# Optimization experiments

Measured on AMD Instinct MI355X. Metric: run time of the kernel, lower is better.

## Reference

```python
import jax, jax.numpy as jnp
import numpy as np
import math

D_MODEL = 256
D_STATE = 16
DT_RANK = math.ceil(D_MODEL / 16)  # 16
WINDOW = 8
B, S = 2, 1024
LN_EPS = 1e-5


def setup_inputs() -> dict:
    key = jax.random.key(0)
    ks = jax.random.split(key, 24)
    d, n, r = D_MODEL, D_STATE, DT_RANK
    sc = lambda fan_in: 1.0 / math.sqrt(fan_in)
    inp = {
        "x": jax.random.normal(ks[0], (B, S, d), jnp.float32),
        # SelectiveSSM params
        "A_log": jnp.log(jnp.abs(jax.random.normal(ks[1], (d, n))) + 1e-4),
        "W_xproj": jax.random.normal(ks[2], (d, r + n)) * sc(d),
        "W_dt": jax.random.normal(ks[3], (r, d)) * sc(r),
        "b_dt": jnp.zeros((d,)),
        "W_C": jax.random.normal(ks[4], (d, n)) * sc(d),
        # LinearAttentionPathway params
        "Wq": jax.random.normal(ks[5], (d, d)) * sc(d),
        "Wk": jax.random.normal(ks[6], (d, d)) * sc(d),
        "Wv": jax.random.normal(ks[7], (d, d)) * sc(d),
        "Wo": jax.random.normal(ks[8], (d, d)) * sc(d),
        "omega": jax.random.normal(ks[9], (d, d)) * 0.5,  # RFF frequencies (buffer)
        # EntropyGate net: Linear(2d+1 -> d), SiLU, Linear(d -> d), Sigmoid
        "Wg1": jax.random.normal(ks[10], (2 * d + 1, d)) * sc(2 * d + 1),
        "bg1": jnp.zeros((d,)),
        "Wg2": jax.random.normal(ks[11], (d, d)) * sc(d),
        "bg2": jnp.zeros((d,)),
        # LayerNorms
        "ln1_g": jnp.ones((d,)), "ln1_b": jnp.zeros((d,)),
        "ln2_g": jnp.ones((d,)), "ln2_b": jnp.zeros((d,)),
        # FFN (dropout is identity in eval)
        "Wf1": jax.random.normal(ks[12], (d, 4 * d)) * sc(d),
        "bf1": jnp.zeros((4 * d,)),
        "Wf2": jax.random.normal(ks[13], (4 * d, d)) * sc(4 * d),
        "bf2": jnp.zeros((d,)),
    }
    return inp


def _layernorm(x, g, b):
    mu = jnp.mean(x, axis=-1, keepdims=True)
    var = jnp.mean((x - mu) ** 2, axis=-1, keepdims=True)
    return (x - mu) / jnp.sqrt(var + LN_EPS) * g + b


def _ssm(x, A_log, W_xproj, W_dt, b_dt, W_C):
    b, s, d = x.shape
    A = -jnp.exp(A_log)                                   # (d, n)
    xp = x @ W_xproj                                      # (b, s, r+n)
    delta = jax.nn.softplus(xp[..., :DT_RANK] @ W_dt + b_dt)  # (b, s, d)
    Bt = xp[..., DT_RANK:]                                # (b, s, n)
    Ct = x @ W_C                                          # (b, s, n)

    def step(h, ins):
        dlt, B_, C_, x_ = ins                             # (b,d),(b,n),(b,n),(b,d)
        A_bar = jnp.exp(dlt[..., None] * A)               # (b, d, n)
        h = A_bar * h + (dlt * x_)[..., None] * B_[:, None, :]
        y = jnp.einsum('bn,bdn->bd', C_, h)
        return h, y

    xs = (delta.transpose(1, 0, 2), Bt.transpose(1, 0, 2),
          Ct.transpose(1, 0, 2), x.transpose(1, 0, 2))
    h0 = jnp.zeros((b, d, D_STATE), x.dtype)
    _, ys = jax.lax.scan(step, h0, xs)                    # (s, b, d)
    return ys.transpose(1, 0, 2)


def _rff(x, omega):
    proj = x @ omega
    scale = math.sqrt(2.0 / D_MODEL)
    return scale * jnp.concatenate([jnp.cos(proj), jnp.sin(proj)], axis=-1)


def _linear_attn(x, Wq, Wk, Wv, Wo, omega):
    b, s, d = x.shape
    Qp = _rff(x @ Wq, omega)                              # (b, s, 2d)
    Kp = _rff(x @ Wk, omega)                              # (b, s, 2d)
    V = x @ Wv                                            # (b, s, d)
    f = 2 * d

    def step(carry, ins):
        Sm, Z = carry                                     # (b,f,d), (b,f)
        q, k, v = ins
        Sm = Sm + k[..., None] * v[:, None, :]
        Z = Z + k
        num = jnp.einsum('bf,bfd->bd', q, Sm)
        den = jnp.sum(q * Z, axis=-1, keepdims=True)
        return (Sm, Z), num / (den + 1e-6)

    xs = (Qp.transpose(1, 0, 2), Kp.transpose(1, 0, 2), V.transpose(1, 0, 2))
    carry0 = (jnp.zeros((b, f, d), x.dtype), jnp.zeros((b, f), x.dtype))
    _, ys = jax.lax.scan(step, carry0, xs)                # (s, b, d)
    return ys.transpose(1, 0, 2) @ Wo


def _entropy(x):
    # H_t over trailing window of token L2-norms; softmax over window.
    m = jnp.linalg.norm(x, axis=-1)                       # (b, s)
    mp = jnp.pad(m, ((0, 0), (WINDOW - 1, 0)), constant_values=-jnp.inf)
    s = m.shape[1]
    # windows[b, t, w]: norms of positions t-W+1..t (padded with -inf)
    windows = jnp.stack([mp[:, i:i + s] for i in range(WINDOW)], axis=-1)
    p = jax.nn.softmax(windows, axis=-1)                  # -inf pads -> p=0
    H = -jnp.sum(p * (jnp.log(p + 1e-9) / jnp.log(2.0)), axis=-1, keepdims=True)
    return H                                              # (b, s, 1)


def reference(x, A_log, W_xproj, W_dt, b_dt, W_C, Wq, Wk, Wv, Wo, omega,
              Wg1, bg1, Wg2, bg2, ln1_g, ln1_b, ln2_g, ln2_b,
              Wf1, bf1, Wf2, bf2):
    residual = x
    y_ssm = _ssm(x, A_log, W_xproj, W_dt, b_dt, W_C)
    y_attn = _linear_attn(x, Wq, Wk, Wv, Wo, omega)
    H = _entropy(x)
    gate_in = jnp.concatenate([y_ssm, y_attn, H], axis=-1)
    g = jax.nn.sigmoid(jax.nn.silu(gate_in @ Wg1 + bg1) @ Wg2 + bg2)
    y_gated = g * y_ssm + (1.0 - g) * y_attn
    h = _layernorm(residual + y_gated, ln1_g, ln1_b)
    ffn = jax.nn.gelu(h @ Wf1 + bf1, approximate=False) @ Wf2 + bf2
    return _layernorm(h + ffn, ln2_g, ln2_b)
```

## Files before the change

### kernel.cpp

```cpp
#include <hip/hip_runtime.h>
#include <math.h>

typedef unsigned short ushort_t;
typedef unsigned int uint_t;
typedef __attribute__((ext_vector_type(8))) short short8;
typedef __attribute__((ext_vector_type(4))) float f32x4;

#define ACT_NONE     0
#define ACT_SOFTPLUS 1
#define ACT_SILU     2
#define ACT_SIGMOID  3
#define ACT_GELU     4
#define ACT_RFF      5
#define ACT_CAUSAL   6

__device__ __forceinline__ ushort_t f2b(float f) {
    union { float f; uint_t u; } v; v.f = f;
    uint_t u = v.u;
    uint_t r = (u + 0x7FFFu + ((u >> 16) & 1u)) >> 16;
    return (ushort_t)r;
}
__device__ __forceinline__ float b2f(ushort_t h) {
    union { uint_t u; float f; } v; v.u = ((uint_t)h) << 16;
    return v.f;
}
__device__ __forceinline__ void split2(float v, ushort_t& h0, ushort_t& h1) {
    h0 = f2b(v); h1 = f2b(v - b2f(h0));
}
__device__ __forceinline__ void split3(float v, ushort_t& h0, ushort_t& h1, ushort_t& h2) {
    h0 = f2b(v); float r1 = v - b2f(h0);
    h1 = f2b(r1); h2 = f2b(r1 - b2f(h1));
}

__device__ __forceinline__ float fast_erf(float x) {
    float ax = fabsf(x);
    float t = 1.f / (1.f + 0.3275911f * ax);
    float poly = t * (0.254829592f + t * (-0.284496736f + t * (1.421413741f
               + t * (-1.453152027f + t * 1.061405429f))));
    float er = 1.f - poly * __expf(-ax * ax);
    return copysignf(er, x);
}

__device__ __forceinline__ float act_apply(float v, int act) {
    switch (act) {
        case ACT_SOFTPLUS: return v > 0.f ? v + __logf(1.f + __expf(-v)) : __logf(1.f + __expf(v));
        case ACT_SILU:     return v / (1.f + __expf(-v));
        case ACT_SIGMOID:  return 1.f / (1.f + __expf(-v));
        case ACT_GELU:     return 0.5f * v * (1.f + fast_erf(v * 0.7071067811865475f));
        default:           return v;
    }
}

#define LDK2 72
#define TSTRIDE 66

struct GJob {
    const ushort_t *A0, *A1, *A2, *B0, *B1, *B2;
    const float* bias;
    float* outF;
    ushort_t *o0, *o1, *o2, *t0, *t1;
    int lda, ldb, ldo, ldob, colOffB, act, ns, K, N;
    int nx, ny, base, zmod;
    int sAb1, sAb2, sBb1, sBb2, sOb, sObB, sTb;
};

template<int NSMAX>
__global__ __launch_bounds__(256)
void gemm_multi(GJob J0, GJob J1, GJob J2, GJob J3, GJob J4)
{
    __shared__ ushort_t sA[NSMAX][64 * LDK2];
    __shared__ ushort_t sB[NSMAX][64 * LDK2];

    GJob J = J0;
    int bid = blockIdx.x;
    if (J4.nx && bid >= J4.base) J = J4;
    else if (J3.nx && bid >= J3.base) J = J3;
    else if (J2.nx && bid >= J2.base) J = J2;
    else if (J1.nx && bid >= J1.base) J = J1;

    int rel = bid - J.base;
    int perz = J.nx * J.ny;
    int bz = rel / perz; rel -= bz * perz;
    int by = rel / J.nx, bx = rel - by * J.nx;
    int zq = bz / J.zmod, zr = bz - zq * J.zmod;

    const ushort_t* As[3] = {J.A0, J.A1, J.A2};
    const ushort_t* Bs[3] = {J.B0, J.B1, J.B2};
    long offA = (long)zq * J.sAb1 + (long)zr * J.sAb2;
    long offB = (long)zq * J.sBb1 + (long)zr * J.sBb2;
    #pragma unroll
    for (int s = 0; s < NSMAX; ++s) { As[s] += offA; Bs[s] += offB; }
    float* outF = J.outF ? J.outF + (long)bz * J.sOb : nullptr;
    ushort_t* o0 = J.o0 ? J.o0 + (long)bz * J.sObB : nullptr;
    ushort_t* o1 = J.o1 ? J.o1 + (long)bz * J.sObB : nullptr;
    ushort_t* o2 = J.o2 ? J.o2 + (long)bz * J.sObB : nullptr;

    const int m0 = by * 64, n0 = bx * 64;
    const int tid = threadIdx.x, lane = tid & 63, wid = tid >> 6;
    const int wr = (wid >> 1) * 32, wc = (wid & 1) * 32;
    const int lr = lane & 15, lk = (lane >> 4) * 8;
    const int rS = tid >> 3, c8 = (tid & 7) * 8;

    uint4 rA[NSMAX][2], rB[NSMAX][2];

    auto LOAD = [&](int k0) {
        #pragma unroll
        for (int s = 0; s < NSMAX; ++s) if (s < J.ns) {
            #pragma unroll
            for (int p = 0; p < 2; ++p) {
                rA[s][p] = *(const uint4*)(As[s] + (long)(m0 + rS + 32 * p) * J.lda + k0 + c8);
                rB[s][p] = *(const uint4*)(Bs[s] + (long)(n0 + rS + 32 * p) * J.ldb + k0 + c8);
            }
        }
    };
    auto STORE = [&]() {
        #pragma unroll
        for (int s = 0; s < NSMAX; ++s) if (s < J.ns) {
            #pragma unroll
            for (int p = 0; p < 2; ++p) {
                *(uint4*)&sA[s][(rS + 32 * p) * LDK2 + c8] = rA[s][p];
                *(uint4*)&sB[s][(rS + 32 * p) * LDK2 + c8] = rB[s][p];
            }
        }
    };

    f32x4 acc[2][2];
    #pragma unroll
    for (int i = 0; i < 2; ++i)
        #pragma unroll
        for (int j = 0; j < 2; ++j)
            acc[i][j] = (f32x4){0.f, 0.f, 0.f, 0.f};

    const int niter = J.K >> 6;
    LOAD(0);
    for (int it = 0; it < niter; ++it) {
        if (it) __syncthreads();
        STORE();
        __syncthreads();
        if (it + 1 < niter) LOAD((it + 1) << 6);
        #pragma unroll
        for (int ks = 0; ks < 2; ++ks) {
            short8 af[NSMAX][2], bg[NSMAX][2];
            #pragma unroll
            for (int s = 0; s < NSMAX; ++s) if (s < J.ns) {
                af[s][0] = *(const short8*)&sA[s][(wr + lr) * LDK2 + ks * 32 + lk];
                af[s][1] = *(const short8*)&sA[s][(wr + 16 + lr) * LDK2 + ks * 32 + lk];
                bg[s][0] = *(const short8*)&sB[s][(wc + lr) * LDK2 + ks * 32 + lk];
                bg[s][1] = *(const short8*)&sB[s][(wc + 16 + lr) * LDK2 + ks * 32 + lk];
            }
            #pragma unroll
            for (int i = 0; i < 2; ++i) {
                #pragma unroll
                for (int j = 0; j < 2; ++j) {
                    acc[i][j] = __builtin_amdgcn_mfma_f32_16x16x32_bf16(af[0][i], bg[0][j], acc[i][j], 0, 0, 0);
                    if constexpr (NSMAX >= 2) if (J.ns >= 2) {
                        acc[i][j] = __builtin_amdgcn_mfma_f32_16x16x32_bf16(af[0][i], bg[1][j], acc[i][j], 0, 0, 0);
                        acc[i][j] = __builtin_amdgcn_mfma_f32_16x16x32_bf16(af[1][i], bg[0][j], acc[i][j], 0, 0, 0);
                    }
                    if constexpr (NSMAX >= 3) if (J.ns >= 3) {
                        acc[i][j] = __builtin_amdgcn_mfma_f32_16x16x32_bf16(af[0][i], bg[2][j], acc[i][j], 0, 0, 0);
                        acc[i][j] = __builtin_amdgcn_mfma_f32_16x16x32_bf16(af[1][i], bg[1][j], acc[i][j], 0, 0, 0);
                        acc[i][j] = __builtin_amdgcn_mfma_f32_16x16x32_bf16(af[2][i], bg[0][j], acc[i][j], 0, 0, 0);
                    }
                }
            }
        }
    }

    ushort_t* sAf = &sA[0][0];
    ushort_t* sBf = &sB[0][0];
    const bool hasT = (J.t0 != nullptr);
    if (hasT) __syncthreads();

    #pragma unroll
    for (int i = 0; i < 2; ++i) {
        #pragma unroll
        for (int j = 0; j < 2; ++j) {
            #pragma unroll
            for (int rr = 0; rr < 4; ++rr) {
                int rl2 = wr + i * 16 + (lane >> 4) * 4 + rr;
                int cl2 = wc + j * 16 + lr;
                int row = m0 + rl2;
                int col = n0 + cl2;
                if (col >= J.N) continue;
                float v = acc[i][j][rr];
                if (J.bias) v += J.bias[col];
                if (J.act == ACT_RFF) {
                    const float sc = 0.08838834764831845f;
                    float sv_, cv_;
                    __sincosf(v, &sv_, &cv_);
                    float cv = sc * cv_, sv = sc * sv_;
                    ushort_t ch = f2b(cv), sh = f2b(sv);
                    ushort_t cL = f2b(cv - b2f(ch)), sL = f2b(sv - b2f(sh));
                    long oc = (long)row * J.ldob + col, os = oc + J.N;
                    o0[oc] = ch; o0[os] = sh;
                    o1[oc] = cL; o1[os] = sL;
                    if (hasT) {
                        sAf[cl2 * TSTRIDE + rl2] = ch;
                        sAf[4224 + cl2 * TSTRIDE + rl2] = cL;
                        sBf[cl2 * TSTRIDE + rl2] = sh;
                        sBf[4224 + cl2 * TSTRIDE + rl2] = sL;
                    }
                    continue;
                }
                if (J.act == ACT_CAUSAL) { if (col > row) v = 0.f; }
                else v = act_apply(v, J.act);
                if (outF) outF[(long)row * J.ldo + col] = v;
                if (o0) {
                    long o = (long)row * J.ldob + J.colOffB + col;
                    ushort_t h0 = f2b(v); o0[o] = h0;
                    if (o1) {
                        float r1 = v - b2f(h0);
                        ushort_t h1 = f2b(r1); o1[o] = h1;
                        if (o2) o2[o] = f2b(r1 - b2f(h1));
                    }
                }
                if (hasT) {
                    ushort_t h0 = f2b(v);
                    sAf[cl2 * TSTRIDE + rl2] = h0;
                    sAf[4224 + cl2 * TSTRIDE + rl2] = f2b(v - b2f(h0));
                }
            }
        }
    }

    if (hasT) {
        __syncthreads();
        int bb = m0 >> 10, tl0 = m0 & 1023;
        int cl = tid >> 2, seg = tid & 3;
        int ngroups = (J.act == ACT_RFF) ? 2 : 1;
        for (int g = 0; g < ngroups; ++g) {
            const ushort_t* th = (g ? sBf : sAf) + cl * TSTRIDE + seg * 16;
            const ushort_t* tl = th + 4224;
            long gcol = (long)(n0 + cl) + (long)g * J.N;
            long addr = (long)bb * J.sTb + gcol * 1024 + tl0 + seg * 16;
            uint_t wh[8], wl[8];
            #pragma unroll
            for (int k2 = 0; k2 < 8; ++k2) {
                wh[k2] = (uint_t)th[2 * k2] | ((uint_t)th[2 * k2 + 1] << 16);
                wl[k2] = (uint_t)tl[2 * k2] | ((uint_t)tl[2 * k2 + 1] << 16);
            }
            *(uint4*)(J.t0 + addr)     = *(uint4*)&wh[0];
            *(uint4*)(J.t0 + addr + 8) = *(uint4*)&wh[4];
            *(uint4*)(J.t1 + addr)     = *(uint4*)&wl[0];
            *(uint4*)(J.t1 + addr + 8) = *(uint4*)&wl[4];
        }
    }
}

#define CONV_BLKS 6400
__global__ __launch_bounds__(256)
void convert_kernel(const float* __restrict__ x, const float* __restrict__ Wxp,
                    const float* __restrict__ Wdt, const float* __restrict__ Wc,
                    const float* __restrict__ Wq, const float* __restrict__ Wk,
                    const float* __restrict__ Wv, const float* __restrict__ Wo,
                    const float* __restrict__ omega, const float* __restrict__ Wg1,
                    const float* __restrict__ Wg2, const float* __restrict__ Wf1,
                    const float* __restrict__ Wf2,
                    ushort_t* x0, ushort_t* x1, ushort_t* x2,
                    ushort_t* omT0, ushort_t* omT1, ushort_t* omT2,
                    ushort_t* Wq0, ushort_t* Wq1, ushort_t* Wq2,
                    ushort_t* Wk0, ushort_t* Wk1, ushort_t* Wk2,
                    ushort_t* WvT0, ushort_t* WvT1, ushort_t* WoT0, ushort_t* WoT1,
                    ushort_t* Wg1T0, ushort_t* Wg1T1, ushort_t* Wg2T0, ushort_t* Wg2T1,
                    ushort_t* Wf1T, ushort_t* Wf2T,
                    ushort_t* WdtT0, ushort_t* WdtT1, ushort_t* WxpP0, ushort_t* WxpP1,
                    ushort_t* WbcT0, ushort_t* WbcT1, float* mbuf)
{
    if (blockIdx.x >= CONV_BLKS) {
        int w = threadIdx.x >> 6, lane = threadIdx.x & 63;
        int token = (blockIdx.x - CONV_BLKS) * 4 + w;
        const float4 v = ((const float4*)(x + (long)token * 256))[lane];
        float s = v.x * v.x + v.y * v.y + v.z * v.z + v.w * v.w;
        #pragma unroll
        for (int msk = 32; msk; msk >>= 1) s += __shfl_xor(s, msk, 64);
        if (lane == 0) mbuf[token] = sqrtf(s);
        return;
    }
    int i = blockIdx.x * 256 + threadIdx.x;
    if (i < 524288) { split3(x[i], x0[i], x1[i], x2[i]); return; }
    i -= 524288;
    if (i < 65536) { int r = i >> 8, c = i & 255; split3(omega[c * 256 + r], omT0[i], omT1[i], omT2[i]); return; }
    i -= 65536;
    if (i < 65536) { split3(Wq[i], Wq0[i], Wq1[i], Wq2[i]); return; }
    i -= 65536;
    if (i < 65536) { split3(Wk[i], Wk0[i], Wk1[i], Wk2[i]); return; }
    i -= 65536;
    if (i < 65536) { int r = i >> 8, c = i & 255; split2(Wv[c * 256 + r], WvT0[i], WvT1[i]); return; }
    i -= 65536;
    if (i < 65536) { int r = i >> 8, c = i & 255; split2(Wo[c * 256 + r], WoT0[i], WoT1[i]); return; }
    i -= 65536;
    if (i < 147456) { int r = i / 576, c = i - r * 576;
                      float v = (c < 513) ? Wg1[c * 256 + r] : 0.f;
                      split2(v, Wg1T0[i], Wg1T1[i]); return; }
    i -= 147456;
    if (i < 65536) { int r = i >> 8, c = i & 255; split2(Wg2[c * 256 + r], Wg2T0[i], Wg2T1[i]); return; }
    i -= 65536;
    if (i < 262144) { int r = i >> 8, c = i & 255; Wf1T[i] = f2b(Wf1[c * 1024 + r]); return; }
    i -= 262144;
    if (i < 262144) { int r = i >> 10, c = i & 1023; Wf2T[i] = f2b(Wf2[c * 256 + r]); return; }
    i -= 262144;
    if (i < 16384) { int m = i >> 6, k = i & 63;
                     float v = (k < 16) ? Wdt[k * 256 + m] : 0.f;
                     split2(v, WdtT0[i], WdtT1[i]); return; }
    i -= 16384;
    if (i < 16384) { int n = i >> 6, k = i & 63;
                     float v = (k < 16) ? Wxp[n * 32 + k] : 0.f;
                     split2(v, WxpP0[i], WxpP1[i]); return; }
    i -= 16384;
    if (i < 16384) { int r = i >> 8, c = i & 255;
                     float v = (r < 16) ? Wxp[c * 32 + 16 + r] : ((r < 32) ? Wc[c * 16 + (r - 16)] : 0.f);
                     split2(v, WbcT0[i], WbcT1[i]); return; }
}

template<int PASS>
__global__ __launch_bounds__(256)
void ssm_pass(const float* __restrict__ x, const float* __restrict__ delta,
              const float* __restrict__ BtCt, const float* __restrict__ A_log,
              float* __restrict__ hend, float* __restrict__ Pst,
              const float* __restrict__ hstart,
              ushort_t* __restrict__ giH, ushort_t* __restrict__ giL)
{
    __shared__ float sd[64][16], sx[64][16], sB[64][16], sC[64][16];
    const int bx = blockIdx.x;
    const int dblk = bx & 15, c = (bx >> 4) & 15, b = bx >> 8;
    const int tid = threadIdx.x;
    const int n = tid & 15, dl = tid >> 4;
    const int d = dblk * 16 + dl;
    #pragma unroll
    for (int it = 0; it < 4; ++it) {
        int i = it * 256 + tid;
        int t = i >> 4, j = i & 15;
        long row = (long)b * 1024 + c * 64 + t;
        sd[t][j] = delta[row * 256 + dblk * 16 + j];
        sx[t][j] = x[row * 256 + dblk * 16 + j];
        sB[t][j] = BtCt[row * 32 + j];
        if (PASS == 3) sC[t][j] = BtCt[row * 32 + 16 + j];
    }
    __syncthreads();
    const float acoef = -__expf(A_log[d * 16 + n]);
    float h = 0.f, P = 1.f;
    if (PASS == 3) h = hstart[((long)(b * 16 + c) << 12) + d * 16 + n];
    for (int t = 0; t < 64; ++t) {
        float dlt = sd[t][dl];
        float a = __expf(dlt * acoef);
        h = a * h + (dlt * sx[t][dl]) * sB[t][n];
        if (PASS == 1) P *= a;
        if (PASS == 3) {
            float part = sC[t][n] * h;
            #pragma unroll
            for (int msk = 8; msk; msk >>= 1) part += __shfl_xor(part, msk, 16);
            if (n == 0) {
                long row = (long)b * 1024 + c * 64 + t;
                ushort_t hh = f2b(part);
                giH[row * 576 + d] = hh;
                giL[row * 576 + d] = f2b(part - b2f(hh));
            }
        }
    }
    if (PASS == 1) {
        long idx = ((long)(b * 16 + c) << 12) + d * 16 + n;
        hend[idx] = h;
        Pst[idx] = P;
    }
}

__global__ void ssm_scan_kernel(const float* __restrict__ hend,
                                const float* __restrict__ Pst,
                                float* __restrict__ hstart,
                                const ushort_t* __restrict__ Kh,
                                const ushort_t* __restrict__ Kl,
                                float* __restrict__ dzc)
{
    int gb = blockIdx.x;
    if (gb < 32) {
        int tid = gb * 256 + threadIdx.x;
        int b = tid >> 12;
        int dn = tid & 4095;
        float hs = 0.f;
        for (int c = 0; c < 16; ++c) {
            long idx = ((long)(b * 16 + c) << 12) + dn;
            hstart[idx] = hs;
            hs = Pst[idx] * hs + hend[idx];
        }
    } else {
        int idx = (gb - 32) * 256 + threadIdx.x;
        int bc = idx >> 9, f = idx & 511;
        float s = 0.f;
        for (int t = 0; t < 128; ++t) {
            long i = ((long)bc * 128 + t) * 512 + f;
            s += b2f(Kh[i]) + b2f(Kl[i]);
        }
        dzc[(long)bc * 512 + f] = s;
    }
}

__global__ void sscan_kernel(const float* __restrict__ dST,
                             ushort_t* __restrict__ STh, ushort_t* __restrict__ STl)
{
    int t = blockIdx.x * 256 + threadIdx.x;
    int b = t >> 17;
    int df = t & 131071;
    float acc = 0.f;
    for (int c = 0; c < 8; ++c) {
        long idx = (long)(b * 8 + c) * 131072 + df;
        ushort_t h = f2b(acc);
        STh[idx] = h;
        STl[idx] = f2b(acc - b2f(h));
        acc += dST[idx];
    }
}

__global__ void attn_finish(const float* __restrict__ scores,
                            const ushort_t* __restrict__ Qh, const ushort_t* __restrict__ Ql,
                            const float* __restrict__ dzc,
                            const float* __restrict__ numA, const float* __restrict__ numB,
                            const float* __restrict__ mbuf,
                            ushort_t* __restrict__ yh, ushort_t* __restrict__ yl,
                            ushort_t* __restrict__ giH, ushort_t* __restrict__ giL)
{
    int token = blockIdx.x;
    int b = token >> 10, tloc = token & 1023;
    int c = tloc >> 7, tin = tloc & 127;
    int bc = b * 8 + c;
    int lane = threadIdx.x;
    const float* srow = scores + ((long)bc * 128 + tin) * 128;
    float s = srow[lane] + srow[lane + 64];
    const ushort_t* qh = Qh + (long)token * 512;
    const ushort_t* ql = Ql + (long)token * 512;
    float q[8];
    #pragma unroll
    for (int j = 0; j < 8; ++j) {
        int f = lane + 64 * j;
        q[j] = b2f(qh[f]) + b2f(ql[f]);
    }
    for (int c2 = 0; c2 < c; ++c2) {
        const float* z = dzc + (long)(b * 8 + c2) * 512;
        #pragma unroll
        for (int j = 0; j < 8; ++j) s += q[j] * z[lane + 64 * j];
    }
    #pragma unroll
    for (int m = 32; m; m >>= 1) s += __shfl_xor(s, m, 64);
    float inv = 1.f / (s + 1e-6f);
    const float* na = numA + (long)token * 256;
    const float* nb = numB + (long)token * 256;
    #pragma unroll
    for (int j = 0; j < 4; ++j) {
        int idx = lane + 64 * j;
        float v = (na[idx] + nb[idx]) * inv;
        ushort_t h = f2b(v);
        yh[(long)token * 256 + idx] = h;
        yl[(long)token * 256 + idx] = f2b(v - b2f(h));
    }
    if (lane == 0) {
        float w[8];
        #pragma unroll
        for (int i = 0; i < 8; ++i) {
            int idx = tloc - 7 + i;
            w[i] = (idx >= 0) ? mbuf[b * 1024 + idx] : -1e30f;
        }
        float mx = w[0];
        #pragma unroll
        for (int i = 1; i < 8; ++i) mx = fmaxf(mx, w[i]);
        float e[8], sum = 0.f;
        #pragma unroll
        for (int i = 0; i < 8; ++i) { e[i] = __expf(w[i] - mx); sum += e[i]; }
        float invs = 1.f / sum, Hv = 0.f;
        #pragma unroll
        for (int i = 0; i < 8; ++i) {
            float p = e[i] * invs;
            Hv -= p * __logf(p + 1e-9f);
        }
        float H = Hv * 1.4426950408889634f;
        ushort_t hh = f2b(H);
        giH[(long)token * 576 + 512] = hh;
        giL[(long)token * 576 + 512] = f2b(H - b2f(hh));
    }
    if (lane < 63) {
        giH[(long)token * 576 + 513 + lane] = 0;
        giL[(long)token * 576 + 513 + lane] = 0;
    }
}

__global__ __launch_bounds__(256)
void ln1_kernel(const float* __restrict__ x, const float* __restrict__ g,
                const ushort_t* __restrict__ giH, const ushort_t* __restrict__ giL,
                const float* __restrict__ gamma, const float* __restrict__ beta,
                float* __restrict__ outF, ushort_t* __restrict__ outB)
{
    __shared__ float red[8];
    long t = blockIdx.x;
    int i = threadIdx.x;
    long idx = t * 256 + i;
    float yssm  = b2f(giH[t * 576 + i])       + b2f(giL[t * 576 + i]);
    float yattn = b2f(giH[t * 576 + 256 + i]) + b2f(giL[t * 576 + 256 + i]);
    float gv = g[idx];
    float v = x[idx] + gv * yssm + (1.f - gv) * yattn;
    float s = v;
    #pragma unroll
    for (int m = 32; m; m >>= 1) s += __shfl_xor(s, m, 64);
    if ((i & 63) == 0) red[i >> 6] = s;
    __syncthreads();
    float mu = (red[0] + red[1] + red[2] + red[3]) * (1.f / 256.f);
    float dv = v - mu;
    float s2 = dv * dv;
    #pragma unroll
    for (int m = 32; m; m >>= 1) s2 += __shfl_xor(s2, m, 64);
    if ((i & 63) == 0) red[4 + (i >> 6)] = s2;
    __syncthreads();
    float var = (red[4] + red[5] + red[6] + red[7]) * (1.f / 256.f);
    float o = dv * rsqrtf(var + 1e-5f) * gamma[i] + beta[i];
    outF[idx] = o;
    outB[idx] = f2b(o);
}

__global__ __launch_bounds__(256)
void ln2_kernel(const float* __restrict__ h, const float* __restrict__ f2,
                const float* __restrict__ gamma, const float* __restrict__ beta,
                float* __restrict__ out)
{
    __shared__ float red[8];
    long t = blockIdx.x;
    int i = threadIdx.x;
    long idx = t * 256 + i;
    float v = h[idx] + f2[idx];
    float s = v;
    #pragma unroll
    for (int m = 32; m; m >>= 1) s += __shfl_xor(s, m, 64);
    if ((i & 63) == 0) red[i >> 6] = s;
    __syncthreads();
    float mu = (red[0] + red[1] + red[2] + red[3]) * (1.f / 256.f);
    float dv = v - mu;
    float s2 = dv * dv;
    #pragma unroll
    for (int m = 32; m; m >>= 1) s2 += __shfl_xor(s2, m, 64);
    if ((i & 63) == 0) red[4 + (i >> 6)] = s2;
    __syncthreads();
    float var = (red[4] + red[5] + red[6] + red[7]) * (1.f / 256.f);
    out[idx] = dv * rsqrtf(var + 1e-5f) * gamma[i] + beta[i];
}


extern "C" void kernel_launch(void* const* d_in, const int* in_sizes, int n_in,
                              void* d_out, int out_size, void* d_ws, size_t ws_size,
                              hipStream_t stream)
{
    const float* x       = (const float*)d_in[0];
    const float* A_log   = (const float*)d_in[1];
    const float* W_xproj = (const float*)d_in[2];
    const float* W_dt    = (const float*)d_in[3];
    const float* b_dt    = (const float*)d_in[4];
    const float* W_C     = (const float*)d_in[5];
    const float* Wq      = (const float*)d_in[6];
    const float* Wk      = (const float*)d_in[7];
    const float* Wv      = (const float*)d_in[8];
    const float* Wo      = (const float*)d_in[9];
    const float* omega   = (const float*)d_in[10];
    const float* Wg1     = (const float*)d_in[11];
    const float* bg1     = (const float*)d_in[12];
    const float* Wg2     = (const float*)d_in[13];
    const float* bg2     = (const float*)d_in[14];
    const float* ln1_g   = (const float*)d_in[15];
    const float* ln1_b   = (const float*)d_in[16];
    const float* ln2_g   = (const float*)d_in[17];
    const float* ln2_b   = (const float*)d_in[18];
    const float* Wf1     = (const float*)d_in[19];
    const float* bf1     = (const float*)d_in[20];
    const float* Wf2     = (const float*)d_in[21];
    const float* bf2     = (const float*)d_in[22];

    char* B = (char*)d_ws;
    float* out = (float*)d_out;
    if (ws_size < (size_t)36216832) return;

    ushort_t* x0      = (ushort_t*)(B + 0);
    ushort_t* x1      = (ushort_t*)(B + 1048576);
    ushort_t* x2      = (ushort_t*)(B + 2097152);
    ushort_t* Qp_hi   = (ushort_t*)(B + 3145728);
    ushort_t* Qp_lo   = (ushort_t*)(B + 5242880);
    ushort_t* Kp_hi   = (ushort_t*)(B + 7340032);
    ushort_t* Kp_lo   = (ushort_t*)(B + 9437184);
    ushort_t* KpT_hi  = (ushort_t*)(B + 11534336);
    ushort_t* KpT_lo  = (ushort_t*)(B + 13631488);
    ushort_t* VT_hi   = (ushort_t*)(B + 15728640);
    ushort_t* VT_lo   = (ushort_t*)(B + 16777216);
    float*    dST_f   = (float*)(B + 17825792);
    float*    delta_f = (float*)(B + 26214400);
    float*    BtCt_f  = (float*)(B + 28311552);
    ushort_t* Wg1T0   = (ushort_t*)(B + 28573696);
    ushort_t* Wg1T1   = (ushort_t*)(B + 28868608);
    ushort_t* Wf1T    = (ushort_t*)(B + 29163520);
    ushort_t* Wf2T    = (ushort_t*)(B + 29687808);
    ushort_t* WxdT0   = (ushort_t*)(B + 30212096);
    ushort_t* WxdT1   = (ushort_t*)(B + 30343168);
    ushort_t* WvT0    = (ushort_t*)(B + 30474240);
    ushort_t* WvT1    = (ushort_t*)(B + 30605312);
    ushort_t* WoT0    = (ushort_t*)(B + 30736384);
    ushort_t* WoT1    = (ushort_t*)(B + 30867456);
    ushort_t* Wg2T0   = (ushort_t*)(B + 30998528);
    ushort_t* Wg2T1   = (ushort_t*)(B + 31129600);
    ushort_t* WdtT0   = (ushort_t*)(B + 31260672);
    ushort_t* WdtT1   = (ushort_t*)(B + 31293440);
    ushort_t* WxpP0   = (ushort_t*)(B + 31326208);
    ushort_t* WxpP1   = (ushort_t*)(B + 31358976);
    ushort_t* WbcT0   = (ushort_t*)(B + 31391744);
    ushort_t* WbcT1   = (ushort_t*)(B + 31424512);
    float*    mbuf    = (float*)(B + 31457280);
    float*    dzc     = (float*)(B + 31465472);
    ushort_t* gatein_hi = (ushort_t*)(B + 31498240);
    ushort_t* gatein_lo = (ushort_t*)(B + 33857536);
    ushort_t* omT0  = (ushort_t*)(B + 17825792);
    ushort_t* omT1  = (ushort_t*)(B + 17956864);
    ushort_t* omT2  = (ushort_t*)(B + 18087936);
    ushort_t* Wq0   = (ushort_t*)(B + 18219008);
    ushort_t* Wq1   = (ushort_t*)(B + 18350080);
    ushort_t* Wq2   = (ushort_t*)(B + 18481152);
    ushort_t* Wk0   = (ushort_t*)(B + 18612224);
    ushort_t* Wk1   = (ushort_t*)(B + 18743296);
    ushort_t* Wk2   = (ushort_t*)(B + 18874368);
    ushort_t* WqoT0 = (ushort_t*)(B + 19005440);
    ushort_t* WqoT1 = (ushort_t*)(B + 19136512);
    ushort_t* WqoT2 = (ushort_t*)(B + 19267584);
    ushort_t* WkoT0 = (ushort_t*)(B + 19398656);
    ushort_t* WkoT1 = (ushort_t*)(B + 19529728);
    ushort_t* WkoT2 = (ushort_t*)(B + 19660800);
    ushort_t* ST_hi = (ushort_t*)(B + 11534336);
    ushort_t* ST_lo = (ushort_t*)(B + 7340032);
    float*    hend   = (float*)(B + 0);
    float*    Pst    = (float*)(B + 524288);
    float*    hstart = (float*)(B + 1048576);
    float*    scores_f  = (float*)(B + 26214400);
    ushort_t* scores_hi = (ushort_t*)(B + 27262976);
    ushort_t* scores_lo = (ushort_t*)(B + 27787264);
    float*    numA_f = (float*)(B + 17825792);
    float*    numB_f = (float*)(B + 19922944);
    ushort_t* g1_hi  = (ushort_t*)(B + 22020096);
    ushort_t* g1_lo  = (ushort_t*)(B + 23068672);
    float*    gbuf_f = (float*)(B + 24117248);
    ushort_t* ypre_hi = (ushort_t*)(B + 7340032);
    ushort_t* ypre_lo = (ushort_t*)(B + 8388608);
    float*    hbuf_f  = (float*)(B + 11534336);
    ushort_t* hbuf_b  = (ushort_t*)(B + 13631488);
    ushort_t* ffn1_b  = (ushort_t*)(B + 3145728);
    float*    ffn2_f  = (float*)(B + 15728640);

    dim3 T256(256);
    GJob jz{};

    convert_kernel<<<dim3(CONV_BLKS + 512), T256, 0, stream>>>(x, W_xproj, W_dt, W_C,
        Wq, Wk, Wv, Wo, omega, Wg1, Wg2, Wf1, Wf2,
        x0, x1, x2, omT0, omT1, omT2, Wq0, Wq1, Wq2, Wk0, Wk1, Wk2,
        WvT0, WvT1, WoT0, WoT1, Wg1T0, Wg1T1, Wg2T0, Wg2T1, Wf1T, Wf2T,
        WdtT0, WdtT1, WxpP0, WxpP1, WbcT0, WbcT1, mbuf);

    {
        GJob a{}; a.A0=omT0; a.A1=omT1; a.A2=omT2; a.B0=Wq0; a.B1=Wq1; a.B2=Wq2;
        a.o0=WqoT0; a.o1=WqoT1; a.o2=WqoT2; a.lda=256; a.ldb=256; a.ldob=256;
        a.act=ACT_NONE; a.ns=3; a.K=256; a.N=256; a.nx=4; a.ny=4; a.base=0; a.zmod=1;
        GJob b = a; b.B0=Wk0; b.B1=Wk1; b.B2=Wk2; b.o0=WkoT0; b.o1=WkoT1; b.o2=WkoT2; b.base=16;
        GJob c{}; c.A0=WdtT0; c.A1=WdtT1; c.B0=WxpP0; c.B1=WxpP1;
        c.o0=WxdT0; c.o1=WxdT1; c.lda=64; c.ldb=64; c.ldob=256;
        c.act=ACT_NONE; c.ns=2; c.K=64; c.N=256; c.nx=4; c.ny=4; c.base=32; c.zmod=1;
        gemm_multi<3><<<dim3(48), T256, 0, stream>>>(a, b, c, jz, jz);
    }
    {
        GJob v{}; v.A0=x0; v.A1=x1; v.B0=WvT0; v.B1=WvT1;
        v.t0=VT_hi; v.t1=VT_lo; v.sTb=262144;
        v.lda=256; v.ldb=256; v.act=ACT_NONE; v.ns=2; v.K=256; v.N=256;
        v.nx=4; v.ny=32; v.base=0; v.zmod=1;
        GJob q{}; q.A0=x0; q.A1=x1; q.A2=x2; q.B0=WqoT0; q.B1=WqoT1; q.B2=WqoT2;
        q.o0=Qp_hi; q.o1=Qp_lo; q.lda=256; q.ldb=256; q.ldob=512;
        q.act=ACT_RFF; q.ns=3; q.K=256; q.N=256; q.nx=4; q.ny=32; q.base=128; q.zmod=1;
        GJob k = q; k.B0=WkoT0; k.B1=WkoT1; k.B2=WkoT2; k.o0=Kp_hi; k.o1=Kp_lo;
        k.t0=KpT_hi; k.t1=KpT_lo; k.sTb=524288; k.base=256;
        GJob bc{}; bc.A0=x0; bc.A1=x1; bc.B0=WbcT0; bc.B1=WbcT1;
        bc.outF=BtCt_f; bc.lda=256; bc.ldb=256; bc.ldo=32;
        bc.act=ACT_NONE; bc.ns=2; bc.K=256; bc.N=32; bc.nx=1; bc.ny=32; bc.base=384; bc.zmod=1;
        GJob dl{}; dl.A0=x0; dl.A1=x1; dl.B0=WxdT0; dl.B1=WxdT1; dl.bias=b_dt;
        dl.outF=delta_f; dl.lda=256; dl.ldb=256; dl.ldo=256;
        dl.act=ACT_SOFTPLUS; dl.ns=2; dl.K=256; dl.N=256; dl.nx=4; dl.ny=32; dl.base=416; dl.zmod=1;
        gemm_multi<3><<<dim3(544), T256, 0, stream>>>(v, q, k, bc, dl);
    }
    ssm_pass<1><<<dim3(512), T256, 0, stream>>>(x, delta_f, BtCt_f, A_log, hend, Pst, nullptr, nullptr, nullptr);
    ssm_scan_kernel<<<dim3(64), T256, 0, stream>>>(hend, Pst, hstart, Kp_hi, Kp_lo, dzc);
    ssm_pass<3><<<dim3(512), T256, 0, stream>>>(x, delta_f, BtCt_f, A_log, nullptr, nullptr, hstart, gatein_hi, gatein_lo);

    {
        GJob d{}; d.A0=VT_hi; d.A1=VT_lo; d.B0=KpT_hi; d.B1=KpT_lo;
        d.outF=dST_f; d.lda=1024; d.ldb=1024; d.ldo=512;
        d.act=ACT_NONE; d.ns=2; d.K=128; d.N=512; d.nx=8; d.ny=4; d.base=0; d.zmod=8;
        d.sAb1=262144; d.sAb2=128; d.sBb1=524288; d.sBb2=128; d.sOb=131072;
        GJob s{}; s.A0=Qp_hi; s.A1=Qp_lo; s.B0=Kp_hi; s.B1=Kp_lo;
        s.outF=scores_f; s.o0=scores_hi; s.o1=scores_lo;
        s.lda=512; s.ldb=512; s.ldo=128; s.ldob=128;
        s.act=ACT_CAUSAL; s.ns=2; s.K=512; s.N=128; s.nx=2; s.ny=2; s.base=512; s.zmod=1;
        s.sAb1=65536; s.sBb1=65536; s.sOb=16384; s.sObB=16384;
        gemm_multi<2><<<dim3(576), T256, 0, stream>>>(d, s, jz, jz, jz);
    }
    sscan_kernel<<<dim3(1024), T256, 0, stream>>>(dST_f, ST_hi, ST_lo);

    {
        GJob a{}; a.A0=scores_hi; a.A1=scores_lo; a.B0=VT_hi; a.B1=VT_lo;
        a.outF=numA_f; a.lda=128; a.ldb=1024; a.ldo=256;
        a.act=ACT_NONE; a.ns=2; a.K=128; a.N=256; a.nx=4; a.ny=2; a.base=0; a.zmod=8;
        a.sAb1=131072; a.sAb2=16384; a.sBb1=262144; a.sBb2=128; a.sOb=32768;
        GJob b{}; b.A0=Qp_hi; b.A1=Qp_lo; b.B0=ST_hi; b.B1=ST_lo;
        b.outF=numB_f; b.lda=512; b.ldb=512; b.ldo=256;
        b.act=ACT_NONE; b.ns=2; b.K=512; b.N=256; b.nx=4; b.ny=2; b.base=128; b.zmod=1;
        b.sAb1=65536; b.sBb1=131072; b.sOb=32768;
        gemm_multi<2><<<dim3(256), T256, 0, stream>>>(a, b, jz, jz, jz);
    }
    attn_finish<<<dim3(2048), dim3(64), 0, stream>>>(scores_f, Qp_hi, Qp_lo, dzc,
        numA_f, numB_f, mbuf, ypre_hi, ypre_lo, gatein_hi, gatein_lo);

    {
        GJob w{}; w.A0=ypre_hi; w.A1=ypre_lo; w.B0=WoT0; w.B1=WoT1;
        w.o0=gatein_hi; w.o1=gatein_lo; w.colOffB=256;
        w.lda=256; w.ldb=256; w.ldob=576;
        w.act=ACT_NONE; w.ns=2; w.K=256; w.N=256; w.nx=4; w.ny=32; w.base=0; w.zmod=1;
        gemm_multi<2><<<dim3(128), T256, 0, stream>>>(w, jz, jz, jz, jz);
    }
    {
        GJob g{}; g.A0=gatein_hi; g.A1=gatein_lo; g.B0=Wg1T0; g.B1=Wg1T1; g.bias=bg1;
        g.o0=g1_hi; g.o1=g1_lo; g.lda=576; g.ldb=576; g.ldob=256;
        g.act=ACT_SILU; g.ns=2; g.K=576; g.N=256; g.nx=4; g.ny=32; g.base=0; g.zmod=1;
        gemm_multi<2><<<dim3(128), T256, 0, stream>>>(g, jz, jz, jz, jz);
    }
    {
        GJob g{}; g.A0=g1_hi; g.A1=g1_lo; g.B0=Wg2T0; g.B1=Wg2T1; g.bias=bg2;
        g.outF=gbuf_f; g.lda=256; g.ldb=256; g.ldo=256;
        g.act=ACT_SIGMOID; g.ns=2; g.K=256; g.N=256; g.nx=4; g.ny=32; g.base=0; g.zmod=1;
        gemm_multi<2><<<dim3(128), T256, 0, stream>>>(g, jz, jz, jz, jz);
    }
    ln1_kernel<<<dim3(2048), T256, 0, stream>>>(x, gbuf_f, gatein_hi, gatein_lo, ln1_g, ln1_b, hbuf_f, hbuf_b);
    {
        GJob f{}; f.A0=hbuf_b; f.B0=Wf1T; f.bias=bf1;
        f.o0=ffn1_b; f.lda=256; f.ldb=256; f.ldob=1024;
        f.act=ACT_GELU; f.ns=1; f.K=256; f.N=1024; f.nx=16; f.ny=32; f.base=0; f.zmod=1;
        gemm_multi<1><<<dim3(512), T256, 0, stream>>>(f, jz, jz, jz, jz);
    }
    {
        GJob f{}; f.A0=ffn1_b; f.B0=Wf2T; f.bias=bf2;
        f.outF=ffn2_f; f.lda=1024; f.ldb=1024; f.ldo=256;
        f.act=ACT_NONE; f.ns=1; f.K=1024; f.N=256; f.nx=4; f.ny=32; f.base=0; f.zmod=1;
        gemm_multi<1><<<dim3(128), T256, 0, stream>>>(f, jz, jz, jz, jz);
    }
    ln2_kernel<<<dim3(2048), T256, 0, stream>>>(hbuf_f, ffn2_f, ln2_g, ln2_b, out);
}
```

Measured before the change: 329.4 us.

## Fold SSM chunk passes into attention GEMM launches and merge scan kernels

Moves the two SSM chunk-scan passes into extra blocks of the independent attention GEMM launches (pass 1 with the dST/scores GEMM, pass 3 with the numA/numB GEMM), and merges the SSM state scan, dzc reduction and ST prefix scan into one kernel. This cuts four kernel launches and lets the latency-bound sequential SSM blocks run alongside GEMM blocks. To avoid aliasing between concurrently running work, the scores and ST_lo buffers move to new workspace regions, which raises the required workspace size. The price is a larger combined kernel with shared LDS sizing and heterogeneous blocks.

```diff
diff --git a/kernel.cpp b/kernel.cpp
--- a/kernel.cpp
+++ b/kernel.cpp
@@ -64,15 +64,75 @@
     int sAb1, sAb2, sBb1, sBb2, sOb, sObB, sTb;
 };
 
-template<int NSMAX>
+struct SJob {
+    const float *x, *delta, *BtCt, *A_log, *hstart;
+    float *hend, *Pst;
+    ushort_t *giH, *giL;
+    int base;
+};
+
+template<int NSMAX, int AUXPASS>
 __global__ __launch_bounds__(256)
-void gemm_multi(GJob J0, GJob J1, GJob J2, GJob J3, GJob J4)
+void gemm_multi(GJob J0, GJob J1, GJob J2, GJob J3, GJob J4, SJob S)
 {
-    __shared__ ushort_t sA[NSMAX][64 * LDK2];
-    __shared__ ushort_t sB[NSMAX][64 * LDK2];
+    __shared__ ushort_t ldsbuf[NSMAX * 2 * 64 * LDK2];
+    ushort_t (*sA)[64 * LDK2] = (ushort_t(*)[64 * LDK2])ldsbuf;
+    ushort_t (*sB)[64 * LDK2] = (ushort_t(*)[64 * LDK2])(ldsbuf + NSMAX * 64 * LDK2);
+
+    int bid = blockIdx.x;
+
+    if constexpr (AUXPASS != 0) {
+        if (bid >= S.base) {
+            const int bx2 = bid - S.base;
+            const int dblk = bx2 & 15, cc = (bx2 >> 4) & 15, bb2 = bx2 >> 8;
+            const int tid2 = threadIdx.x;
+            const int nn = tid2 & 15, dl = tid2 >> 4;
+            const int dd = dblk * 16 + dl;
+            float* sd  = (float*)ldsbuf;
+            float* sx2 = sd + 1024;
+            float* sB2 = sx2 + 1024;
+            float* sC2 = sB2 + 1024;
+            #pragma unroll
+            for (int it = 0; it < 4; ++it) {
+                int i2 = it * 256 + tid2;
+                int t2 = i2 >> 4, j2 = i2 & 15;
+                long row = (long)bb2 * 1024 + cc * 64 + t2;
+                sd[t2 * 16 + j2]  = S.delta[row * 256 + dblk * 16 + j2];
+                sx2[t2 * 16 + j2] = S.x[row * 256 + dblk * 16 + j2];
+                sB2[t2 * 16 + j2] = S.BtCt[row * 32 + j2];
+                if (AUXPASS == 3) sC2[t2 * 16 + j2] = S.BtCt[row * 32 + 16 + j2];
+            }
+            __syncthreads();
+            const float acoef = -__expf(S.A_log[dd * 16 + nn]);
+            float h = 0.f, P = 1.f;
+            if (AUXPASS == 3) h = S.hstart[((long)(bb2 * 16 + cc) << 12) + dd * 16 + nn];
+            for (int t2 = 0; t2 < 64; ++t2) {
+                float dlt = sd[t2 * 16 + dl];
+                float a2 = __expf(dlt * acoef);
+                h = a2 * h + (dlt * sx2[t2 * 16 + dl]) * sB2[t2 * 16 + nn];
+                if (AUXPASS == 1) P *= a2;
+                if (AUXPASS == 3) {
+                    float part = sC2[t2 * 16 + nn] * h;
+                    #pragma unroll
+                    for (int msk = 8; msk; msk >>= 1) part += __shfl_xor(part, msk, 16);
+                    if (nn == 0) {
+                        long row = (long)bb2 * 1024 + cc * 64 + t2;
+                        ushort_t hh = f2b(part);
+                        S.giH[row * 576 + dd] = hh;
+                        S.giL[row * 576 + dd] = f2b(part - b2f(hh));
+                    }
+                }
+            }
+            if (AUXPASS == 1) {
+                long idx = ((long)(bb2 * 16 + cc) << 12) + dd * 16 + nn;
+                S.hend[idx] = h;
+                S.Pst[idx] = P;
+            }
+            return;
+        }
+    }
 
     GJob J = J0;
-    int bid = blockIdx.x;
     if (J4.nx && bid >= J4.base) J = J4;
     else if (J3.nx && bid >= J3.base) J = J3;
     else if (J2.nx && bid >= J2.base) J = J2;
@@ -313,64 +373,12 @@
                      split2(v, WbcT0[i], WbcT1[i]); return; }
 }
 
-template<int PASS>
-__global__ __launch_bounds__(256)
-void ssm_pass(const float* __restrict__ x, const float* __restrict__ delta,
-              const float* __restrict__ BtCt, const float* __restrict__ A_log,
-              float* __restrict__ hend, float* __restrict__ Pst,
-              const float* __restrict__ hstart,
-              ushort_t* __restrict__ giH, ushort_t* __restrict__ giL)
-{
-    __shared__ float sd[64][16], sx[64][16], sB[64][16], sC[64][16];
-    const int bx = blockIdx.x;
-    const int dblk = bx & 15, c = (bx >> 4) & 15, b = bx >> 8;
-    const int tid = threadIdx.x;
-    const int n = tid & 15, dl = tid >> 4;
-    const int d = dblk * 16 + dl;
-    #pragma unroll
-    for (int it = 0; it < 4; ++it) {
-        int i = it * 256 + tid;
-        int t = i >> 4, j = i & 15;
-        long row = (long)b * 1024 + c * 64 + t;
-        sd[t][j] = delta[row * 256 + dblk * 16 + j];
-        sx[t][j] = x[row * 256 + dblk * 16 + j];
-        sB[t][j] = BtCt[row * 32 + j];
-        if (PASS == 3) sC[t][j] = BtCt[row * 32 + 16 + j];
-    }
-    __syncthreads();
-    const float acoef = -__expf(A_log[d * 16 + n]);
-    float h = 0.f, P = 1.f;
-    if (PASS == 3) h = hstart[((long)(b * 16 + c) << 12) + d * 16 + n];
-    for (int t = 0; t < 64; ++t) {
-        float dlt = sd[t][dl];
-        float a = __expf(dlt * acoef);
-        h = a * h + (dlt * sx[t][dl]) * sB[t][n];
-        if (PASS == 1) P *= a;
-        if (PASS == 3) {
-            float part = sC[t][n] * h;
-            #pragma unroll
-            for (int msk = 8; msk; msk >>= 1) part += __shfl_xor(part, msk, 16);
-            if (n == 0) {
-                long row = (long)b * 1024 + c * 64 + t;
-                ushort_t hh = f2b(part);
-                giH[row * 576 + d] = hh;
-                giL[row * 576 + d] = f2b(part - b2f(hh));
-            }
-        }
-    }
-    if (PASS == 1) {
-        long idx = ((long)(b * 16 + c) << 12) + d * 16 + n;
-        hend[idx] = h;
-        Pst[idx] = P;
-    }
-}
-
-__global__ void ssm_scan_kernel(const float* __restrict__ hend,
-                                const float* __restrict__ Pst,
-                                float* __restrict__ hstart,
-                                const ushort_t* __restrict__ Kh,
-                                const ushort_t* __restrict__ Kl,
-                                float* __restrict__ dzc)
+__global__ void scan_mix(const float* __restrict__ hend, const float* __restrict__ Pst,
+                         float* __restrict__ hstart,
+                         const ushort_t* __restrict__ Kh, const ushort_t* __restrict__ Kl,
+                         float* __restrict__ dzc,
+                         const float* __restrict__ dST,
+                         ushort_t* __restrict__ STh, ushort_t* __restrict__ STl)
 {
     int gb = blockIdx.x;
     if (gb < 32) {
@@ -383,7 +391,7 @@
             hstart[idx] = hs;
             hs = Pst[idx] * hs + hend[idx];
         }
-    } else {
+    } else if (gb < 64) {
         int idx = (gb - 32) * 256 + threadIdx.x;
         int bc = idx >> 9, f = idx & 511;
         float s = 0.f;
@@ -392,22 +400,19 @@
             s += b2f(Kh[i]) + b2f(Kl[i]);
         }
         dzc[(long)bc * 512 + f] = s;
-    }
-}
-
-__global__ void sscan_kernel(const float* __restrict__ dST,
-                             ushort_t* __restrict__ STh, ushort_t* __restrict__ STl)
-{
-    int t = blockIdx.x * 256 + threadIdx.x;
-    int b = t >> 17;
-    int df = t & 131071;
-    float acc = 0.f;
-    for (int c = 0; c < 8; ++c) {
-        long idx = (long)(b * 8 + c) * 131072 + df;
-        ushort_t h = f2b(acc);
-        STh[idx] = h;
-        STl[idx] = f2b(acc - b2f(h));
-        acc += dST[idx];
+    } else {
+        int t = (gb - 64) * 256 + threadIdx.x;
+        int b = t >> 17;
+        int df = t & 131071;
+        float acc = 0.f;
+        for (int c = 0; c < 8; ++c) {
+            long idx = (long)(b * 8 + c) * 131072 + df;
+            float v = dST[idx];
+            ushort_t h = f2b(acc);
+            STh[idx] = h;
+            STl[idx] = f2b(acc - b2f(h));
+            acc += v;
+        }
     }
 }
 
@@ -571,7 +576,7 @@
 
     char* B = (char*)d_ws;
     float* out = (float*)d_out;
-    if (ws_size < (size_t)36216832) return;
+    if (ws_size < (size_t)42778624) return;
 
     ushort_t* x0      = (ushort_t*)(B + 0);
     ushort_t* x1      = (ushort_t*)(B + 1048576);
@@ -609,6 +614,10 @@
     float*    dzc     = (float*)(B + 31465472);
     ushort_t* gatein_hi = (ushort_t*)(B + 31498240);
     ushort_t* gatein_lo = (ushort_t*)(B + 33857536);
+    ushort_t* ST_lo   = (ushort_t*)(B + 36216832);
+    float*    scores_f  = (float*)(B + 40411136);
+    ushort_t* scores_hi = (ushort_t*)(B + 41459712);
+    ushort_t* scores_lo = (ushort_t*)(B + 41984000);
     ushort_t* omT0  = (ushort_t*)(B + 17825792);
     ushort_t* omT1  = (ushort_t*)(B + 17956864);
     ushort_t* omT2  = (ushort_t*)(B + 18087936);
@@ -625,13 +634,9 @@
     ushort_t* WkoT1 = (ushort_t*)(B + 19529728);
     ushort_t* WkoT2 = (ushort_t*)(B + 19660800);
     ushort_t* ST_hi = (ushort_t*)(B + 11534336);
-    ushort_t* ST_lo = (ushort_t*)(B + 7340032);
     float*    hend   = (float*)(B + 0);
     float*    Pst    = (float*)(B + 524288);
     float*    hstart = (float*)(B + 1048576);
-    float*    scores_f  = (float*)(B + 26214400);
-    ushort_t* scores_hi = (ushort_t*)(B + 27262976);
-    ushort_t* scores_lo = (ushort_t*)(B + 27787264);
     float*    numA_f = (float*)(B + 17825792);
     float*    numB_f = (float*)(B + 19922944);
     ushort_t* g1_hi  = (ushort_t*)(B + 22020096);
@@ -646,6 +651,7 @@
 
     dim3 T256(256);
     GJob jz{};
+    SJob sz{};
 
     convert_kernel<<<dim3(CONV_BLKS + 512), T256, 0, stream>>>(x, W_xproj, W_dt, W_C,
         Wq, Wk, Wv, Wo, omega, Wg1, Wg2, Wf1, Wf2,
@@ -661,7 +667,7 @@
         GJob c{}; c.A0=WdtT0; c.A1=WdtT1; c.B0=WxpP0; c.B1=WxpP1;
         c.o0=WxdT0; c.o1=WxdT1; c.lda=64; c.ldb=64; c.ldob=256;
         c.act=ACT_NONE; c.ns=2; c.K=64; c.N=256; c.nx=4; c.ny=4; c.base=32; c.zmod=1;
-        gemm_multi<3><<<dim3(48), T256, 0, stream>>>(a, b, c, jz, jz);
+        gemm_multi<3,0><<<dim3(48), T256, 0, stream>>>(a, b, c, jz, jz, sz);
     }
     {
         GJob v{}; v.A0=x0; v.A1=x1; v.B0=WvT0; v.B1=WvT1;
@@ -679,12 +685,8 @@
         GJob dl{}; dl.A0=x0; dl.A1=x1; dl.B0=WxdT0; dl.B1=WxdT1; dl.bias=b_dt;
         dl.outF=delta_f; dl.lda=256; dl.ldb=256; dl.ldo=256;
         dl.act=ACT_SOFTPLUS; dl.ns=2; dl.K=256; dl.N=256; dl.nx=4; dl.ny=32; dl.base=416; dl.zmod=1;
-        gemm_multi<3><<<dim3(544), T256, 0, stream>>>(v, q, k, bc, dl);
-    }
-    ssm_pass<1><<<dim3(512), T256, 0, stream>>>(x, delta_f, BtCt_f, A_log, hend, Pst, nullptr, nullptr, nullptr);
-    ssm_scan_kernel<<<dim3(64), T256, 0, stream>>>(hend, Pst, hstart, Kp_hi, Kp_lo, dzc);
-    ssm_pass<3><<<dim3(512), T256, 0, stream>>>(x, delta_f, BtCt_f, A_log, nullptr, nullptr, hstart, gatein_hi, gatein_lo);
-
+        gemm_multi<3,0><<<dim3(544), T256, 0, stream>>>(v, q, k, bc, dl, sz);
+    }
     {
         GJob d{}; d.A0=VT_hi; d.A1=VT_lo; d.B0=KpT_hi; d.B1=KpT_lo;
         d.outF=dST_f; d.lda=1024; d.ldb=1024; d.ldo=512;
@@ -695,10 +697,12 @@
         s.lda=512; s.ldb=512; s.ldo=128; s.ldob=128;
         s.act=ACT_CAUSAL; s.ns=2; s.K=512; s.N=128; s.nx=2; s.ny=2; s.base=512; s.zmod=1;
         s.sAb1=65536; s.sBb1=65536; s.sOb=16384; s.sObB=16384;
-        gemm_multi<2><<<dim3(576), T256, 0, stream>>>(d, s, jz, jz, jz);
-    }
-    sscan_kernel<<<dim3(1024), T256, 0, stream>>>(dST_f, ST_hi, ST_lo);
-
+        SJob s1{}; s1.x=x; s1.delta=delta_f; s1.BtCt=BtCt_f; s1.A_log=A_log;
+        s1.hend=hend; s1.Pst=Pst; s1.base=576;
+        gemm_multi<2,1><<<dim3(1088), T256, 0, stream>>>(d, s, jz, jz, jz, s1);
+    }
+    scan_mix<<<dim3(1088), T256, 0, stream>>>(hend, Pst, hstart, Kp_hi, Kp_lo, dzc,
+                                              dST_f, ST_hi, ST_lo);
     {
         GJob a{}; a.A0=scores_hi; a.A1=scores_lo; a.B0=VT_hi; a.B1=VT_lo;
         a.outF=numA_f; a.lda=128; a.ldb=1024; a.ldo=256;
@@ -708,42 +712,43 @@
         b.outF=numB_f; b.lda=512; b.ldb=512; b.ldo=256;
         b.act=ACT_NONE; b.ns=2; b.K=512; b.N=256; b.nx=4; b.ny=2; b.base=128; b.zmod=1;
         b.sAb1=65536; b.sBb1=131072; b.sOb=32768;
-        gemm_multi<2><<<dim3(256), T256, 0, stream>>>(a, b, jz, jz, jz);
+        SJob s3{}; s3.x=x; s3.delta=delta_f; s3.BtCt=BtCt_f; s3.A_log=A_log;
+        s3.hstart=hstart; s3.giH=gatein_hi; s3.giL=gatein_lo; s3.base=256;
+        gemm_multi<2,3><<<dim3(768), T256, 0, stream>>>(a, b, jz, jz, jz, s3);
     }
     attn_finish<<<dim3(2048), dim3(64), 0, stream>>>(scores_f, Qp_hi, Qp_lo, dzc,
         numA_f, numB_f, mbuf, ypre_hi, ypre_lo, gatein_hi, gatein_lo);
-
     {
         GJob w{}; w.A0=ypre_hi; w.A1=ypre_lo; w.B0=WoT0; w.B1=WoT1;
         w.o0=gatein_hi; w.o1=gatein_lo; w.colOffB=256;
         w.lda=256; w.ldb=256; w.ldob=576;
         w.act=ACT_NONE; w.ns=2; w.K=256; w.N=256; w.nx=4; w.ny=32; w.base=0; w.zmod=1;
-        gemm_multi<2><<<dim3(128), T256, 0, stream>>>(w, jz, jz, jz, jz);
+        gemm_multi<2,0><<<dim3(128), T256, 0, stream>>>(w, jz, jz, jz, jz, sz);
     }
     {
         GJob g{}; g.A0=gatein_hi; g.A1=gatein_lo; g.B0=Wg1T0; g.B1=Wg1T1; g.bias=bg1;
         g.o0=g1_hi; g.o1=g1_lo; g.lda=576; g.ldb=576; g.ldob=256;
         g.act=ACT_SILU; g.ns=2; g.K=576; g.N=256; g.nx=4; g.ny=32; g.base=0; g.zmod=1;
-        gemm_multi<2><<<dim3(128), T256, 0, stream>>>(g, jz, jz, jz, jz);
+        gemm_multi<2,0><<<dim3(128), T256, 0, stream>>>(g, jz, jz, jz, jz, sz);
     }
     {
         GJob g{}; g.A0=g1_hi; g.A1=g1_lo; g.B0=Wg2T0; g.B1=Wg2T1; g.bias=bg2;
         g.outF=gbuf_f; g.lda=256; g.ldb=256; g.ldo=256;
         g.act=ACT_SIGMOID; g.ns=2; g.K=256; g.N=256; g.nx=4; g.ny=32; g.base=0; g.zmod=1;
-        gemm_multi<2><<<dim3(128), T256, 0, stream>>>(g, jz, jz, jz, jz);
+        gemm_multi<2,0><<<dim3(128), T256, 0, stream>>>(g, jz, jz, jz, jz, sz);
     }
     ln1_kernel<<<dim3(2048), T256, 0, stream>>>(x, gbuf_f, gatein_hi, gatein_lo, ln1_g, ln1_b, hbuf_f, hbuf_b);
     {
         GJob f{}; f.A0=hbuf_b; f.B0=Wf1T; f.bias=bf1;
         f.o0=ffn1_b; f.lda=256; f.ldb=256; f.ldob=1024;
         f.act=ACT_GELU; f.ns=1; f.K=256; f.N=1024; f.nx=16; f.ny=32; f.base=0; f.zmod=1;
-        gemm_multi<1><<<dim3(512), T256, 0, stream>>>(f, jz, jz, jz, jz);
+        gemm_multi<1,0><<<dim3(512), T256, 0, stream>>>(f, jz, jz, jz, jz, sz);
     }
     {
         GJob f{}; f.A0=ffn1_b; f.B0=Wf2T; f.bias=bf2;
         f.outF=ffn2_f; f.lda=1024; f.ldb=1024; f.ldo=256;
         f.act=ACT_NONE; f.ns=1; f.K=1024; f.N=256; f.nx=4; f.ny=32; f.base=0; f.zmod=1;
-        gemm_multi<1><<<dim3(128), T256, 0, stream>>>(f, jz, jz, jz, jz);
+        gemm_multi<1,0><<<dim3(128), T256, 0, stream>>>(f, jz, jz, jz, jz, sz);
     }
     ln2_kernel<<<dim3(2048), T256, 0, stream>>>(hbuf_f, ffn2_f, ln2_g, ln2_b, out);
 }
```

New measurement: 311.8 us, median of 3. -5.4%, faster.
